# Performance work log

Hardware: AMD Instinct MI355X
Metric: run time of the kernel (lower is better)

Reference implementation:

```python
import jax, jax.numpy as jnp
import numpy as np

NBIT = 8
QMAX = 2 ** (NBIT - 1) - 1  # 127, symmetric 8-bit range


def _sym_scale(x):
    # symmetric_linear_quantization_params: scale = max|x| / (2^(b-1)-1)
    return jnp.max(jnp.abs(x)) / QMAX


def setup_inputs() -> dict:
    key = jax.random.key(0)
    k1, k2, k3 = jax.random.split(key, 3)
    B, DIN, DOUT = 8192, 2048, 8192
    x = jax.random.normal(k1, (B, DIN), jnp.float32)
    weight = jax.random.normal(k2, (DOUT, DIN), jnp.float32) * 0.02
    bias = jax.random.normal(k3, (DOUT,), jnp.float32) * 0.01
    return {"x": x, "weight": weight, "bias": bias}


def reference(x, weight, bias):
    # --- QuantAct 1: symmetric 8-bit activation quantization ---
    s_a = _sym_scale(x)                                   # scalar act scale
    x_int = jnp.clip(jnp.round(x / s_a), -QMAX, QMAX)     # int8 values in fp32
    # --- QuantLinear: per-output-channel 8-bit weight quant + integer GEMM ---
    s_w = jnp.max(jnp.abs(weight), axis=1) / QMAX         # [DOUT] weight scales
    w_int = jnp.clip(jnp.round(weight / s_w[:, None]), -QMAX, QMAX)
    s_b = s_w * s_a                                        # output/bias scale [DOUT]
    b_int = jnp.round(bias / s_b)
    out_int = x_int @ w_int.T + b_int                      # [B, DOUT] int accumulation
    out = out_int * s_b                                    # dequantize
    # --- QuantAct 2: requantize output, symmetric 8-bit ---
    s_o = _sym_scale(out)
    out_q = jnp.clip(jnp.round(out / s_o), -QMAX, QMAX) * s_o
    return out_q
```

## Files before the change

kernel.cpp:

```cpp
#include <hip/hip_runtime.h>
#include <stdint.h>

#define B_DIM 8192
#define DIN   2048
#define DOUT  8192
#define NKT   (DIN / 128)

typedef int  v4i __attribute__((ext_vector_type(4)));
typedef char c8  __attribute__((ext_vector_type(8)));

__device__ __forceinline__ void gload_lds16(const void* g, void* l) {
  __builtin_amdgcn_global_load_lds(
      (const __attribute__((address_space(1))) void*)g,
      (__attribute__((address_space(3))) void*)l, 16, 0, 0);
}

__device__ __forceinline__ float wave_max(float m) {
#pragma unroll
  for (int off = 32; off; off >>= 1) m = fmaxf(m, __shfl_xor(m, off, 64));
  return m;
}

__global__ void k_init(unsigned int* p) {
  p[0] = 0u;
  p[1] = 0u;
}

__global__ __launch_bounds__(256) void k_absmax(const float4* __restrict__ x,
                                                int n4,
                                                unsigned int* __restrict__ out_bits) {
  int idx = blockIdx.x * blockDim.x + threadIdx.x;
  int stride = gridDim.x * blockDim.x;
  float m = 0.f;
  for (int i = idx; i < n4; i += stride) {
    float4 v = x[i];
    m = fmaxf(m, fabsf(v.x));
    m = fmaxf(m, fabsf(v.y));
    m = fmaxf(m, fabsf(v.z));
    m = fmaxf(m, fabsf(v.w));
  }
  m = wave_max(m);
  __shared__ float red[4];
  if ((threadIdx.x & 63) == 0) red[threadIdx.x >> 6] = m;
  __syncthreads();
  if (threadIdx.x == 0) {
    m = fmaxf(fmaxf(red[0], red[1]), fmaxf(red[2], red[3]));
    atomicMax(out_bits, __float_as_uint(m));
  }
}

__global__ void k_quant_x(const float* __restrict__ x, c8* __restrict__ xq,
                          int n8, const unsigned int* __restrict__ sa_bits) {
  int i = blockIdx.x * blockDim.x + threadIdx.x;
  if (i >= n8) return;
  float s_a = __uint_as_float(*sa_bits) / 127.0f;
  const float4* p = (const float4*)(x + (size_t)i * 8);
  float4 v0 = p[0], v1 = p[1];
  float vv[8] = {v0.x, v0.y, v0.z, v0.w, v1.x, v1.y, v1.z, v1.w};
  c8 q;
#pragma unroll
  for (int j = 0; j < 8; ++j) {
    float r = fminf(fmaxf(rintf(vv[j] / s_a), -127.f), 127.f);
    q[j] = (char)(int)r;
  }
  xq[i] = q;
}

__global__ __launch_bounds__(256) void k_quant_w(const float* __restrict__ w,
                                                 c8* __restrict__ wq,
                                                 float* __restrict__ s_w) {
  int row = blockIdx.x;
  int tid = threadIdx.x;
  const float4* wr = (const float4*)(w + (size_t)row * DIN);
  float4 v0 = wr[tid * 2], v1 = wr[tid * 2 + 1];
  float vv[8] = {v0.x, v0.y, v0.z, v0.w, v1.x, v1.y, v1.z, v1.w};
  float m = 0.f;
#pragma unroll
  for (int j = 0; j < 8; ++j) m = fmaxf(m, fabsf(vv[j]));
  m = wave_max(m);
  __shared__ float wmax[4];
  if ((tid & 63) == 0) wmax[tid >> 6] = m;
  __syncthreads();
  m = fmaxf(fmaxf(wmax[0], wmax[1]), fmaxf(wmax[2], wmax[3]));
  float s = m / 127.0f;
  if (tid == 0) s_w[row] = s;
  c8 q;
#pragma unroll
  for (int j = 0; j < 8; ++j) {
    float r = fminf(fmaxf(rintf(vv[j] / s), -127.f), 127.f);
    q[j] = (char)(int)r;
  }
  wq[(size_t)row * (DIN / 8) + tid] = q;
}

__global__ __launch_bounds__(512) void k_gemm8(
    const char* __restrict__ Aq, const char* __restrict__ Bq,
    const float* __restrict__ s_w, const float* __restrict__ bias,
    const unsigned int* __restrict__ sa_bits, float* __restrict__ out,
    unsigned int* __restrict__ omax_bits) {
  __shared__ __align__(16) char lds[131072];

  const int tid = threadIdx.x;
  const int lane = tid & 63;
  const int wave = tid >> 6;
  const int wm = wave >> 2;
  const int wn = wave & 3;

  const int orig = blockIdx.x;
  const int xcd = orig & 7;
  const int k = orig >> 3;
  const int bx = (xcd & 3) * 8 + (k & 7);
  const int by = (xcd >> 2) * 16 + (k >> 3);
  const int row0 = by * 256, col0 = bx * 256;

  const size_t srcOff =
      (size_t)(tid >> 3) * DIN + 16 * ((tid & 7) ^ ((tid >> 3) & 7));
  const char* aS = Aq + (size_t)row0 * DIN + srcOff;
  const char* bS = Bq + (size_t)col0 * DIN + srcOff;

  auto STAGE1 = [&](int kt, int isB, int q) {
    if (kt >= NKT) kt = NKT - 2 + (kt & 1);
    const int slot = kt & 1;
    const char* src = (isB ? bS : aS) + (size_t)(q * 64) * DIN + (size_t)kt * 128;
    gload_lds16(src, &lds[slot * 65536 + isB * 32768 + q * 8192 + tid * 16]);
  };

  v4i acc[2][4][4];
#pragma unroll
  for (int mh = 0; mh < 2; ++mh)
#pragma unroll
    for (int mf = 0; mf < 4; ++mf)
#pragma unroll
      for (int nf = 0; nf < 4; ++nf) acc[mh][mf][nf] = (v4i){0, 0, 0, 0};

  const int fr = lane & 15;
  const int kg = lane >> 4;
  const int lp = fr * 128 + 16 * (kg ^ (fr & 7));
  v4i b_[4];

#define PH(SLOT, KS, MH, SKT, SISB, SQA, SQB)                                \
  do {                                                                       \
    STAGE1(SKT, SISB, SQA);                                                  \
    STAGE1(SKT, SISB, SQB);                                                  \
    v4i a_[4];                                                               \
    const int ab = (SLOT) * 65536 + wm * 16384 + (MH) * 8192 + lp;           \
    const int bb = (SLOT) * 65536 + 32768 + wn * 8192 + lp;                  \
    if (!(MH)) b_[0] = *(const v4i*)&lds[bb ^ ((KS) * 64)];                  \
    _Pragma("unroll") for (int mf = 0; mf < 4; ++mf) a_[mf] =                \
        *(const v4i*)&lds[(ab + mf * 2048) ^ ((KS) * 64)];                   \
    if (!(MH)) {                                                             \
      _Pragma("unroll") for (int nf = 1; nf < 4; ++nf) b_[nf] =              \
          *(const v4i*)&lds[(bb + nf * 2048) ^ ((KS) * 64)];                 \
    }                                                                        \
    asm volatile("s_waitcnt vmcnt(4)" ::: "memory");                         \
    _Pragma("unroll") for (int nf = 0; nf < 4; ++nf)                         \
        _Pragma("unroll") for (int mf = 0; mf < 4; ++mf) acc[MH][mf][nf] =   \
        __builtin_amdgcn_mfma_i32_16x16x64_i8(a_[mf], b_[nf],                \
                                              acc[MH][mf][nf], 0, 0, 0);     \
    __builtin_amdgcn_s_barrier();                                            \
  } while (0)

  STAGE1(0, 0, 0);
  STAGE1(0, 0, 2);
  STAGE1(0, 0, 1);
  STAGE1(0, 0, 3);
  STAGE1(0, 1, 0);
  STAGE1(0, 1, 1);
  STAGE1(0, 1, 2);
  STAGE1(0, 1, 3);
  STAGE1(1, 1, 0);
  STAGE1(1, 1, 1);
  asm volatile("s_waitcnt vmcnt(2)" ::: "memory");
  __builtin_amdgcn_s_barrier();

#pragma unroll 1
  for (int i = 0; i < NKT / 2; ++i) {
    const int t1 = 2 * i + 1, t2 = 2 * i + 2, t3 = 2 * i + 3;
    PH(0, 0, 0, t1, 1, 2, 3);
    PH(0, 0, 1, t1, 0, 0, 2);
    PH(0, 1, 0, t1, 0, 1, 3);
    PH(0, 1, 1, t2, 1, 0, 1);
    PH(1, 0, 0, t2, 1, 2, 3);
    PH(1, 0, 1, t2, 0, 0, 2);
    PH(1, 1, 0, t2, 0, 1, 3);
    PH(1, 1, 1, t3, 1, 0, 1);
  }
#undef PH

  float s_a = __uint_as_float(*sa_bits) / 127.0f;
  float lmax = 0.f;
#pragma unroll
  for (int nf = 0; nf < 4; ++nf) {
    int col = col0 + wn * 64 + nf * 16 + fr;
    float sw = s_w[col];
    float sb = sw * s_a;
    float bint = rintf(bias[col] / sb);
#pragma unroll
    for (int mh = 0; mh < 2; ++mh)
#pragma unroll
      for (int mf = 0; mf < 4; ++mf) {
        int rbase = row0 + wm * 128 + mh * 64 + mf * 16 + (lane >> 4) * 4;
#pragma unroll
        for (int r = 0; r < 4; ++r) {
          float o = ((float)acc[mh][mf][nf][r] + bint) * sb;
          out[(size_t)(rbase + r) * DOUT + col] = o;
          lmax = fmaxf(lmax, fabsf(o));
        }
      }
  }
  lmax = wave_max(lmax);
  asm volatile("s_waitcnt vmcnt(0)" ::: "memory");
  __syncthreads();
  float* red = (float*)lds;
  if (lane == 0) red[wave] = lmax;
  __syncthreads();
  if (tid == 0) {
    float m = 0.f;
#pragma unroll
    for (int w2 = 0; w2 < 8; ++w2) m = fmaxf(m, red[w2]);
    atomicMax(omax_bits, __float_as_uint(m));
  }
}

__global__ void k_requant(float4* __restrict__ out, int n4,
                          const unsigned int* __restrict__ omax_bits) {
  float s_o = __uint_as_float(*omax_bits) / 127.0f;
  int idx = blockIdx.x * blockDim.x + threadIdx.x;
  int stride = gridDim.x * blockDim.x;
  for (int i = idx; i < n4; i += stride) {
    float4 v = out[i];
    v.x = fminf(fmaxf(rintf(v.x / s_o), -127.f), 127.f) * s_o;
    v.y = fminf(fmaxf(rintf(v.y / s_o), -127.f), 127.f) * s_o;
    v.z = fminf(fmaxf(rintf(v.z / s_o), -127.f), 127.f) * s_o;
    v.w = fminf(fmaxf(rintf(v.w / s_o), -127.f), 127.f) * s_o;
    out[i] = v;
  }
}

extern "C" void kernel_launch(void* const* d_in, const int* in_sizes, int n_in,
                              void* d_out, int out_size, void* d_ws,
                              size_t ws_size, hipStream_t stream) {
  const float* x = (const float*)d_in[0];
  const float* w = (const float*)d_in[1];
  const float* bias = (const float*)d_in[2];
  float* out = (float*)d_out;
  char* ws = (char*)d_ws;

  unsigned int* absbits = (unsigned int*)ws;
  float* s_w = (float*)(ws + 512);
  char* xq = ws + 65536;
  char* wq = ws + 65536 + (size_t)B_DIM * DIN;

  k_init<<<1, 1, 0, stream>>>(absbits);
  k_absmax<<<1024, 256, 0, stream>>>((const float4*)x, B_DIM * DIN / 4, absbits);
  k_quant_x<<<(B_DIM * DIN / 8) / 256, 256, 0, stream>>>(x, (c8*)xq,
                                                         B_DIM * DIN / 8, absbits);
  k_quant_w<<<DOUT, 256, 0, stream>>>(w, (c8*)wq, s_w);
  k_gemm8<<<1024, 512, 0, stream>>>(xq, wq, s_w, bias, absbits, out, absbits + 1);
  k_requant<<<4096, 256, 0, stream>>>((float4*)out, B_DIM * DOUT / 4, absbits + 1);
}
```

Measured before the change: 303.7 us.

## Stage GEMM tiles through registers instead of direct global-to-LDS loads

```diff
diff --git a/kernel.cpp b/kernel.cpp
--- a/kernel.cpp
+++ b/kernel.cpp
@@ -119,10 +119,17 @@
   const char* bS = Bq + (size_t)col0 * DIN + srcOff;
 
   auto STAGE1 = [&](int kt, int isB, int q) {
+    const char* src = (isB ? bS : aS) + (size_t)(q * 64) * DIN + (size_t)kt * 128;
+    gload_lds16(src, &lds[(kt & 1) * 65536 + isB * 32768 + q * 8192 + tid * 16]);
+  };
+  auto LOADU = [&](int kt, int isB, int q, v4i* dst) {
     if (kt >= NKT) kt = NKT - 2 + (kt & 1);
-    const int slot = kt & 1;
     const char* src = (isB ? bS : aS) + (size_t)(q * 64) * DIN + (size_t)kt * 128;
-    gload_lds16(src, &lds[slot * 65536 + isB * 32768 + q * 8192 + tid * 16]);
+    *dst = *(const v4i*)src;
+  };
+  auto WRITEU = [&](int kt, int isB, int q, const v4i* v) {
+    if (kt >= NKT) kt = NKT - 2 + (kt & 1);
+    *(v4i*)&lds[(kt & 1) * 65536 + isB * 32768 + q * 8192 + tid * 16] = *v;
   };
 
   v4i acc[2][4][4];
@@ -137,26 +144,30 @@
   const int kg = lane >> 4;
   const int lp = fr * 128 + 16 * (kg ^ (fr & 7));
   v4i b_[4];
-
-#define PH(SLOT, KS, MH, SKT, SISB, SQA, SQB)                                \
+  v4i sA0, sA1, sB0, sB1;
+
+#define PH(SLOT, KS, MH, LKT, LISB, LQA, LQB, WKT, WISB, WQA, WQB, L0, L1,   \
+           W0, W1)                                                           \
   do {                                                                       \
-    STAGE1(SKT, SISB, SQA);                                                  \
-    STAGE1(SKT, SISB, SQB);                                                  \
+    LOADU(LKT, LISB, LQA, &L0);                                              \
+    LOADU(LKT, LISB, LQB, &L1);                                              \
+    asm volatile("s_waitcnt vmcnt(2)" ::: "memory");                         \
+    WRITEU(WKT, WISB, WQA, &W0);                                             \
+    WRITEU(WKT, WISB, WQB, &W1);                                             \
     v4i a_[4];                                                               \
     const int ab = (SLOT) * 65536 + wm * 16384 + (MH) * 8192 + lp;           \
     const int bb = (SLOT) * 65536 + 32768 + wn * 8192 + lp;                  \
-    if (!(MH)) b_[0] = *(const v4i*)&lds[bb ^ ((KS) * 64)];                  \
+    if (!(MH)) {                                                             \
+      _Pragma("unroll") for (int nf = 0; nf < 4; ++nf) b_[nf] =              \
+          *(const v4i*)&lds[(bb + nf * 2048) ^ ((KS) * 64)];                 \
+    }                                                                        \
     _Pragma("unroll") for (int mf = 0; mf < 4; ++mf) a_[mf] =                \
         *(const v4i*)&lds[(ab + mf * 2048) ^ ((KS) * 64)];                   \
-    if (!(MH)) {                                                             \
-      _Pragma("unroll") for (int nf = 1; nf < 4; ++nf) b_[nf] =              \
-          *(const v4i*)&lds[(bb + nf * 2048) ^ ((KS) * 64)];                 \
-    }                                                                        \
-    asm volatile("s_waitcnt vmcnt(4)" ::: "memory");                         \
     _Pragma("unroll") for (int nf = 0; nf < 4; ++nf)                         \
         _Pragma("unroll") for (int mf = 0; mf < 4; ++mf) acc[MH][mf][nf] =   \
         __builtin_amdgcn_mfma_i32_16x16x64_i8(a_[mf], b_[nf],                \
                                               acc[MH][mf][nf], 0, 0, 0);     \
+    asm volatile("s_waitcnt lgkmcnt(0)" ::: "memory");                       \
     __builtin_amdgcn_s_barrier();                                            \
   } while (0)
 
@@ -170,20 +181,22 @@
   STAGE1(0, 1, 3);
   STAGE1(1, 1, 0);
   STAGE1(1, 1, 1);
+  LOADU(1, 1, 2, &sA0);
+  LOADU(1, 1, 3, &sA1);
   asm volatile("s_waitcnt vmcnt(2)" ::: "memory");
   __builtin_amdgcn_s_barrier();
 
 #pragma unroll 1
   for (int i = 0; i < NKT / 2; ++i) {
     const int t1 = 2 * i + 1, t2 = 2 * i + 2, t3 = 2 * i + 3;
-    PH(0, 0, 0, t1, 1, 2, 3);
-    PH(0, 0, 1, t1, 0, 0, 2);
-    PH(0, 1, 0, t1, 0, 1, 3);
-    PH(0, 1, 1, t2, 1, 0, 1);
-    PH(1, 0, 0, t2, 1, 2, 3);
-    PH(1, 0, 1, t2, 0, 0, 2);
-    PH(1, 1, 0, t2, 0, 1, 3);
-    PH(1, 1, 1, t3, 1, 0, 1);
+    PH(0, 0, 0, t1, 0, 0, 2, t1, 1, 2, 3, sB0, sB1, sA0, sA1);
+    PH(0, 0, 1, t1, 0, 1, 3, t1, 0, 0, 2, sA0, sA1, sB0, sB1);
+    PH(0, 1, 0, t2, 1, 0, 1, t1, 0, 1, 3, sB0, sB1, sA0, sA1);
+    PH(0, 1, 1, t2, 1, 2, 3, t2, 1, 0, 1, sA0, sA1, sB0, sB1);
+    PH(1, 0, 0, t2, 0, 0, 2, t2, 1, 2, 3, sB0, sB1, sA0, sA1);
+    PH(1, 0, 1, t2, 0, 1, 3, t2, 0, 0, 2, sA0, sA1, sB0, sB1);
+    PH(1, 1, 0, t3, 1, 0, 1, t2, 0, 1, 3, sB0, sB1, sA0, sA1);
+    PH(1, 1, 1, t3, 1, 2, 3, t3, 1, 0, 1, sA0, sA1, sB0, sB1);
   }
 #undef PH
 
@@ -209,7 +222,7 @@
       }
   }
   lmax = wave_max(lmax);
-  asm volatile("s_waitcnt vmcnt(0)" ::: "memory");
+  asm volatile("s_waitcnt vmcnt(0) lgkmcnt(0)" ::: "memory");
   __syncthreads();
   float* red = (float*)lds;
   if (lane == 0) red[wave] = lmax;
```

Measured after the change: 332.8 us. 9.6% more time.

## Stage B tile through registers instead of direct global-to-LDS loads

Applied to the files above, without the earlier changes.

```diff
diff --git a/kernel.cpp b/kernel.cpp
--- a/kernel.cpp
+++ b/kernel.cpp
@@ -120,9 +120,16 @@
 
   auto STAGE1 = [&](int kt, int isB, int q) {
     if (kt >= NKT) kt = NKT - 2 + (kt & 1);
-    const int slot = kt & 1;
     const char* src = (isB ? bS : aS) + (size_t)(q * 64) * DIN + (size_t)kt * 128;
-    gload_lds16(src, &lds[slot * 65536 + isB * 32768 + q * 8192 + tid * 16]);
+    gload_lds16(src, &lds[(kt & 1) * 65536 + isB * 32768 + q * 8192 + tid * 16]);
+  };
+  auto LOADU = [&](int kt, int q, v4i* dst) {
+    if (kt >= NKT) kt = NKT - 2 + (kt & 1);
+    *dst = *(const v4i*)(bS + (size_t)(q * 64) * DIN + (size_t)kt * 128);
+  };
+  auto WRITEU = [&](int kt, int q, const v4i* v) {
+    if (kt >= NKT) kt = NKT - 2 + (kt & 1);
+    *(v4i*)&lds[(kt & 1) * 65536 + 32768 + q * 8192 + tid * 16] = *v;
   };
 
   v4i acc[2][4][4];
@@ -137,26 +144,62 @@
   const int kg = lane >> 4;
   const int lp = fr * 128 + 16 * (kg ^ (fr & 7));
   v4i b_[4];
-
-#define PH(SLOT, KS, MH, SKT, SISB, SQA, SQB)                                \
-  do {                                                                       \
-    STAGE1(SKT, SISB, SQA);                                                  \
-    STAGE1(SKT, SISB, SQB);                                                  \
+  v4i sX0, sX1, sY0, sY1;
+
+#define READS_B(SLOT, KS)                                                    \
+  do {                                                                       \
+    const int bb = (SLOT) * 65536 + 32768 + wn * 8192 + lp;                  \
+    _Pragma("unroll") for (int nf = 0; nf < 4; ++nf) b_[nf] =                \
+        *(const v4i*)&lds[(bb + nf * 2048) ^ ((KS) * 64)];                   \
+  } while (0)
+#define MFMA_BLK(SLOT, KS, MH)                                               \
+  do {                                                                       \
     v4i a_[4];                                                               \
     const int ab = (SLOT) * 65536 + wm * 16384 + (MH) * 8192 + lp;           \
-    const int bb = (SLOT) * 65536 + 32768 + wn * 8192 + lp;                  \
-    if (!(MH)) b_[0] = *(const v4i*)&lds[bb ^ ((KS) * 64)];                  \
     _Pragma("unroll") for (int mf = 0; mf < 4; ++mf) a_[mf] =                \
         *(const v4i*)&lds[(ab + mf * 2048) ^ ((KS) * 64)];                   \
-    if (!(MH)) {                                                             \
-      _Pragma("unroll") for (int nf = 1; nf < 4; ++nf) b_[nf] =              \
-          *(const v4i*)&lds[(bb + nf * 2048) ^ ((KS) * 64)];                 \
-    }                                                                        \
-    asm volatile("s_waitcnt vmcnt(4)" ::: "memory");                         \
     _Pragma("unroll") for (int nf = 0; nf < 4; ++nf)                         \
         _Pragma("unroll") for (int mf = 0; mf < 4; ++mf) acc[MH][mf][nf] =   \
         __builtin_amdgcn_mfma_i32_16x16x64_i8(a_[mf], b_[nf],                \
                                               acc[MH][mf][nf], 0, 0, 0);     \
+  } while (0)
+
+#define PH1(SLOT, WKT, W0, W1)                                               \
+  do {                                                                       \
+    asm volatile("s_waitcnt vmcnt(0)" ::: "memory");                         \
+    WRITEU(WKT, 2, &W0);                                                     \
+    WRITEU(WKT, 3, &W1);                                                     \
+    READS_B(SLOT, 0);                                                        \
+    MFMA_BLK(SLOT, 0, 0);                                                    \
+    asm volatile("s_waitcnt lgkmcnt(0)" ::: "memory");                       \
+    __builtin_amdgcn_s_barrier();                                            \
+  } while (0)
+#define PH2(SLOT, AKT)                                                       \
+  do {                                                                       \
+    STAGE1(AKT, 0, 0);                                                       \
+    STAGE1(AKT, 0, 2);                                                       \
+    MFMA_BLK(SLOT, 0, 1);                                                    \
+    __builtin_amdgcn_s_barrier();                                            \
+  } while (0)
+#define PH3(SLOT, LKT, L0, L1, AKT)                                          \
+  do {                                                                       \
+    LOADU(LKT, 0, &L0);                                                      \
+    LOADU(LKT, 1, &L1);                                                      \
+    STAGE1(AKT, 0, 1);                                                       \
+    STAGE1(AKT, 0, 3);                                                       \
+    READS_B(SLOT, 1);                                                        \
+    MFMA_BLK(SLOT, 1, 0);                                                    \
+    __builtin_amdgcn_s_barrier();                                            \
+  } while (0)
+#define PH4(SLOT, LKT, L0, L1, WKT, W0, W1)                                  \
+  do {                                                                       \
+    LOADU(LKT, 2, &L0);                                                      \
+    LOADU(LKT, 3, &L1);                                                      \
+    asm volatile("s_waitcnt vmcnt(4)" ::: "memory");                         \
+    WRITEU(WKT, 0, &W0);                                                     \
+    WRITEU(WKT, 1, &W1);                                                     \
+    MFMA_BLK(SLOT, 1, 1);                                                    \
+    asm volatile("s_waitcnt lgkmcnt(0)" ::: "memory");                       \
     __builtin_amdgcn_s_barrier();                                            \
   } while (0)
 
@@ -170,22 +213,29 @@
   STAGE1(0, 1, 3);
   STAGE1(1, 1, 0);
   STAGE1(1, 1, 1);
+  LOADU(1, 2, &sY0);
+  LOADU(1, 3, &sY1);
   asm volatile("s_waitcnt vmcnt(2)" ::: "memory");
   __builtin_amdgcn_s_barrier();
 
 #pragma unroll 1
   for (int i = 0; i < NKT / 2; ++i) {
     const int t1 = 2 * i + 1, t2 = 2 * i + 2, t3 = 2 * i + 3;
-    PH(0, 0, 0, t1, 1, 2, 3);
-    PH(0, 0, 1, t1, 0, 0, 2);
-    PH(0, 1, 0, t1, 0, 1, 3);
-    PH(0, 1, 1, t2, 1, 0, 1);
-    PH(1, 0, 0, t2, 1, 2, 3);
-    PH(1, 0, 1, t2, 0, 0, 2);
-    PH(1, 1, 0, t2, 0, 1, 3);
-    PH(1, 1, 1, t3, 1, 0, 1);
-  }
-#undef PH
+    PH1(0, t1, sY0, sY1);
+    PH2(0, t1);
+    PH3(0, t2, sX0, sX1, t1);
+    PH4(0, t2, sY0, sY1, t2, sX0, sX1);
+    PH1(1, t2, sY0, sY1);
+    PH2(1, t2);
+    PH3(1, t3, sX0, sX1, t2);
+    PH4(1, t3, sY0, sY1, t3, sX0, sX1);
+  }
+#undef PH1
+#undef PH2
+#undef PH3
+#undef PH4
+#undef READS_B
+#undef MFMA_BLK
 
   float s_a = __uint_as_float(*sa_bits) / 127.0f;
   float lmax = 0.f;
@@ -209,7 +259,7 @@
       }
   }
   lmax = wave_max(lmax);
-  asm volatile("s_waitcnt vmcnt(0)" ::: "memory");
+  asm volatile("s_waitcnt vmcnt(0) lgkmcnt(0)" ::: "memory");
   __syncthreads();
   float* red = (float*)lds;
   if (lane == 0) red[wave] = lmax;
```

Result: slower. 327.9 us (+8.0%).

## Simplify int8 GEMM main loop to per-tile double buffering with full drain

Applied to the files above, without the earlier changes.

```diff
diff --git a/kernel.cpp b/kernel.cpp
--- a/kernel.cpp
+++ b/kernel.cpp
@@ -138,21 +138,18 @@
   const int lp = fr * 128 + 16 * (kg ^ (fr & 7));
   v4i b_[4];
 
-#define PH(SLOT, KS, MH, SKT, SISB, SQA, SQB)                                \
+#define READS_B(SLOT, KS)                                                    \
   do {                                                                       \
-    STAGE1(SKT, SISB, SQA);                                                  \
-    STAGE1(SKT, SISB, SQB);                                                  \
+    const int bb = (SLOT) * 65536 + 32768 + wn * 8192 + lp;                  \
+    _Pragma("unroll") for (int nf = 0; nf < 4; ++nf) b_[nf] =                \
+        *(const v4i*)&lds[(bb + nf * 2048) ^ ((KS) * 64)];                   \
+  } while (0)
+#define MFMA_BLK(SLOT, KS, MH)                                               \
+  do {                                                                       \
     v4i a_[4];                                                               \
     const int ab = (SLOT) * 65536 + wm * 16384 + (MH) * 8192 + lp;           \
-    const int bb = (SLOT) * 65536 + 32768 + wn * 8192 + lp;                  \
-    if (!(MH)) b_[0] = *(const v4i*)&lds[bb ^ ((KS) * 64)];                  \
     _Pragma("unroll") for (int mf = 0; mf < 4; ++mf) a_[mf] =                \
         *(const v4i*)&lds[(ab + mf * 2048) ^ ((KS) * 64)];                   \
-    if (!(MH)) {                                                             \
-      _Pragma("unroll") for (int nf = 1; nf < 4; ++nf) b_[nf] =              \
-          *(const v4i*)&lds[(bb + nf * 2048) ^ ((KS) * 64)];                 \
-    }                                                                        \
-    asm volatile("s_waitcnt vmcnt(4)" ::: "memory");                         \
     _Pragma("unroll") for (int nf = 0; nf < 4; ++nf)                         \
         _Pragma("unroll") for (int mf = 0; mf < 4; ++mf) acc[MH][mf][nf] =   \
         __builtin_amdgcn_mfma_i32_16x16x64_i8(a_[mf], b_[nf],                \
@@ -161,31 +158,50 @@
   } while (0)
 
   STAGE1(0, 0, 0);
+  STAGE1(0, 0, 1);
   STAGE1(0, 0, 2);
-  STAGE1(0, 0, 1);
   STAGE1(0, 0, 3);
   STAGE1(0, 1, 0);
   STAGE1(0, 1, 1);
   STAGE1(0, 1, 2);
   STAGE1(0, 1, 3);
-  STAGE1(1, 1, 0);
-  STAGE1(1, 1, 1);
-  asm volatile("s_waitcnt vmcnt(2)" ::: "memory");
+  asm volatile("s_waitcnt vmcnt(0)" ::: "memory");
   __builtin_amdgcn_s_barrier();
 
 #pragma unroll 1
-  for (int i = 0; i < NKT / 2; ++i) {
-    const int t1 = 2 * i + 1, t2 = 2 * i + 2, t3 = 2 * i + 3;
-    PH(0, 0, 0, t1, 1, 2, 3);
-    PH(0, 0, 1, t1, 0, 0, 2);
-    PH(0, 1, 0, t1, 0, 1, 3);
-    PH(0, 1, 1, t2, 1, 0, 1);
-    PH(1, 0, 0, t2, 1, 2, 3);
-    PH(1, 0, 1, t2, 0, 0, 2);
-    PH(1, 1, 0, t2, 0, 1, 3);
-    PH(1, 1, 1, t3, 1, 0, 1);
-  }
-#undef PH
+  for (int t = 0; t < NKT; ++t) {
+    const int S = t & 1, tn = t + 1;
+    STAGE1(tn, 0, 0);
+    STAGE1(tn, 0, 1);
+    STAGE1(tn, 0, 2);
+    STAGE1(tn, 0, 3);
+    READS_B(S, 0);
+    MFMA_BLK(S, 0, 0);
+    STAGE1(tn, 1, 0);
+    STAGE1(tn, 1, 1);
+    STAGE1(tn, 1, 2);
+    STAGE1(tn, 1, 3);
+    MFMA_BLK(S, 0, 1);
+    READS_B(S, 1);
+    MFMA_BLK(S, 1, 0);
+    {
+      v4i a_[4];
+      const int ab = S * 65536 + wm * 16384 + 8192 + lp;
+#pragma unroll
+      for (int mf = 0; mf < 4; ++mf)
+        a_[mf] = *(const v4i*)&lds[(ab + mf * 2048) ^ 64];
+#pragma unroll
+      for (int nf = 0; nf < 4; ++nf)
+#pragma unroll
+        for (int mf = 0; mf < 4; ++mf)
+          acc[1][mf][nf] = __builtin_amdgcn_mfma_i32_16x16x64_i8(
+              a_[mf], b_[nf], acc[1][mf][nf], 0, 0, 0);
+      asm volatile("s_waitcnt vmcnt(0)" ::: "memory");
+      __builtin_amdgcn_s_barrier();
+    }
+  }
+#undef READS_B
+#undef MFMA_BLK
 
   float s_a = __uint_as_float(*sa_bits) / 127.0f;
   float lmax = 0.f;
```

After: 313.2 us. 1.03x slower.
